# Kernel optimization log

Hardware: AMD Instinct MI355X
Metric: run time of the kernel (lower is better)

Reference implementation:

```python
import jax, jax.numpy as jnp
import numpy as np

HEADS = 8
HEAD_DIM = 32
DIM = 256        # embed_dim; inner_dim = HEADS*HEAD_DIM = 256
DEPTH = 2
MLP_DIM = 1024
GRID_H, GRID_W = 64, 64
CELL_DIM = 15    # pe(0) + in(3) + out(3) + hidden(9)
PE_IN = 3        # cell_pe_patch_dim + cell_in_patch_dim
UPDATE_DIM = 12  # cell_out(3) + hidden(9)
BATCH = 8


def layer_norm(x, g, b, eps=1e-5):
    m = jnp.mean(x, axis=-1, keepdims=True)
    v = jnp.var(x, axis=-1, keepdims=True)
    return (x - m) * jax.lax.rsqrt(v + eps) * g + b


def vit_positional_encoding(n, dim):
    pos = jnp.arange(n, dtype=jnp.float32)[:, None]
    div = jnp.exp(jnp.arange(0, dim, 2, dtype=jnp.float32) * (-np.log(10000.0) / dim))
    pe = jnp.zeros((n, dim), dtype=jnp.float32)
    pe = pe.at[:, 0::2].set(jnp.sin(pos * div)).at[:, 1::2].set(jnp.cos(pos * div))
    return pe[None]  # [1, n, dim]


def localize(x, H, W):
    # x: [b, heads, n, d] with n = H*W. Gather circular 3x3 neighbourhood per position
    # (equivalent to circular pad + one-hot conv in the torch LocalizeAttention).
    b, nh, n, d = x.shape
    y = x.reshape(b, nh, H, W, d)
    neigh = [jnp.roll(y, (1 - ki, 1 - kj), axis=(2, 3)) for ki in range(3) for kj in range(3)]
    return jnp.stack(neigh, axis=4).reshape(b, nh, n, 9, d)  # [b, h, n, 9, d]


def setup_inputs() -> dict:
    key = jax.random.key(0)
    ks = jax.random.split(key, 20)
    d = {}
    d['cells'] = jax.random.normal(ks[0], (BATCH, CELL_DIM, GRID_H, GRID_W), dtype=jnp.float32)
    s = 0.02
    d['We'] = jax.random.normal(ks[1], (CELL_DIM, DIM), jnp.float32) * s
    d['be'] = jnp.zeros((DIM,), jnp.float32)
    d['ln1_g'] = jnp.ones((DEPTH, DIM), jnp.float32)
    d['ln1_b'] = jnp.zeros((DEPTH, DIM), jnp.float32)
    d['Wqkv'] = jax.random.normal(ks[2], (DEPTH, DIM, 3 * HEADS * HEAD_DIM), jnp.float32) * s
    d['Wo'] = jax.random.normal(ks[3], (DEPTH, HEADS * HEAD_DIM, DIM), jnp.float32) * s
    d['bo'] = jnp.zeros((DEPTH, DIM), jnp.float32)
    d['ln2_g'] = jnp.ones((DEPTH, DIM), jnp.float32)
    d['ln2_b'] = jnp.zeros((DEPTH, DIM), jnp.float32)
    d['W1'] = jax.random.normal(ks[4], (DEPTH, DIM, MLP_DIM), jnp.float32) * s
    d['b1'] = jnp.zeros((DEPTH, MLP_DIM), jnp.float32)
    d['W2'] = jax.random.normal(ks[5], (DEPTH, MLP_DIM, DIM), jnp.float32) * s
    d['b2'] = jnp.zeros((DEPTH, DIM), jnp.float32)
    d['lnh_g'] = jnp.ones((DIM,), jnp.float32)
    d['lnh_b'] = jnp.zeros((DIM,), jnp.float32)
    # NOTE: torch zero-inits mlp_head; we use small random weights so the output is nontrivial.
    d['Wh'] = jax.random.normal(ks[6], (DIM, UPDATE_DIM), jnp.float32) * s
    d['bh'] = jnp.zeros((UPDATE_DIM,), jnp.float32)
    return d


def reference(cells, We, be, ln1_g, ln1_b, Wqkv, Wo, bo, ln2_g, ln2_b,
              W1, b1, W2, b2, lnh_g, lnh_b, Wh, bh):
    b, c, H, W = cells.shape
    n = H * W
    x = cells.reshape(b, c, n).transpose(0, 2, 1)           # b n c
    x = x @ We + be                                         # cell_to_embedding
    x = x + vit_positional_encoding(n, x.shape[-1])
    scale = HEAD_DIM ** -0.5
    for l in range(DEPTH):
        y = layer_norm(x, ln1_g[l], ln1_b[l])
        qkv = y @ Wqkv[l]                                   # b n 3*inner
        q, k, v = jnp.split(qkv, 3, axis=-1)
        split_heads = lambda t: t.reshape(b, n, HEADS, HEAD_DIM).transpose(0, 2, 1, 3)
        q, k, v = split_heads(q), split_heads(k), split_heads(v)  # b h n d
        kl = localize(k, H, W)                              # b h n 9 d
        vl = localize(v, H, W)
        dots = jnp.einsum('bhnd,bhnkd->bhnk', q, kl) * scale
        attn = jax.nn.softmax(dots, axis=-1)
        out = jnp.einsum('bhnk,bhnkd->bhnd', attn, vl)
        out = out.transpose(0, 2, 1, 3).reshape(b, n, HEADS * HEAD_DIM)
        x = out @ Wo[l] + bo[l] + x                         # attention + residual
        y = layer_norm(x, ln2_g[l], ln2_b[l])
        y = jax.nn.gelu(y @ W1[l] + b1[l], approximate=False) @ W2[l] + b2[l]
        x = x + y                                           # ffn + residual
    upd = layer_norm(x, lnh_g, lnh_b) @ Wh + bh             # b n UPDATE_DIM
    upd = upd.transpose(0, 2, 1).reshape(b, UPDATE_DIM, H, W)
    # update_rate = 1.0 -> deterministic branch: cells[:, PE_IN:] + update
    updated = cells[:, PE_IN:] + upd
    return jnp.concatenate([cells[:, :PE_IN], updated], axis=1)
```

## Files before the change

kernel.cpp:

```cpp
#include <hip/hip_runtime.h>
#include <hip/hip_bf16.h>
#include <math.h>

#define HEADS 8
#define HEAD_DIM 32
#define DIM 256
#define MLP_DIM 1024
#define NTOK 4096
#define BATCH 8
#define M_TOK (BATCH*NTOK)
#define CELL_DIM 15
#define PE_IN 3
#define UPD 12
#define HME ((size_t)M_TOK*32)

typedef __attribute__((ext_vector_type(8))) short bf16x8;
typedef __attribute__((ext_vector_type(4))) float f32x4;

static __device__ __forceinline__ unsigned short f2bf(float f) {
    __hip_bfloat16 h = __float2bfloat16(f);
    union { __hip_bfloat16 h; unsigned short u; } cv; cv.h = h; return cv.u;
}
static __device__ __forceinline__ void gload_lds16(const unsigned short* g, unsigned short* l) {
    __builtin_amdgcn_global_load_lds(
        (const __attribute__((address_space(1))) void*)g,
        (__attribute__((address_space(3))) void*)l, 16, 0, 0);
}
static __device__ __forceinline__ float gelu_fast(float v) {
    return v / (1.f + __expf(-1.59576912f * (v + 0.044715f * v * v * v)));
}

__global__ __launch_bounds__(256) void k_embed(const float* __restrict__ cells,
        const float* __restrict__ We, const float* __restrict__ be,
        const float* __restrict__ g, const float* __restrict__ bln,
        float* __restrict__ x, unsigned short* __restrict__ y) {
    __shared__ float red[8];
    int tok = blockIdx.x;
    int d = threadIdx.x;
    int b = tok >> 12, n = tok & 4095;
    const float* cb = cells + (size_t)b * CELL_DIM * NTOK + n;
    float acc = 0.f;
#pragma unroll
    for (int c = 0; c < CELL_DIM; ++c)
        acc += cb[c * NTOK] * We[c * DIM + d];
    int i = d >> 1;
    float freq = expf(-logf(10000.f) * (float)(2 * i) / (float)DIM);
    float ph = (float)n * freq;
    float pe = (d & 1) ? cosf(ph) : sinf(ph);
    float v = acc + be[d] + pe;
    x[(size_t)tok * DIM + d] = v;
    float s = v, ss = v * v;
#pragma unroll
    for (int off = 32; off; off >>= 1) { s += __shfl_xor(s, off); ss += __shfl_xor(ss, off); }
    int wave = d >> 6, lane = d & 63;
    if (lane == 0) { red[wave] = s; red[4 + wave] = ss; }
    __syncthreads();
    float stot = red[0] + red[1] + red[2] + red[3];
    float sstot = red[4] + red[5] + red[6] + red[7];
    float mean = stot * (1.f / DIM);
    float rstd = rsqrtf(sstot * (1.f / DIM) - mean * mean + 1e-5f);
    y[(size_t)tok * DIM + d] = f2bf((v - mean) * rstd * g[d] + bln[d]);
}

__global__ __launch_bounds__(256) void k_prep(const float* __restrict__ Wqkv,
        const float* __restrict__ Wo, const float* __restrict__ W1,
        const float* __restrict__ W2, const float* __restrict__ Wh,
        unsigned short* __restrict__ wT) {
    int seg = blockIdx.y;
    int idx = blockIdx.x * 256 + threadIdx.x;
    if (seg == 8) {
        if (idx >= 16 * 256) return;
        int u = idx >> 8, k = idx & 255;
        wT[1572864 + idx] = (u < UPD) ? f2bf(Wh[(size_t)k * UPD + u]) : (unsigned short)0;
        return;
    }
    int l = seg >> 2, mat = seg & 3;
    const float* src; int kwSh, Nw; size_t ooff;
    switch (mat) {
        case 0: src = Wqkv + (size_t)l * 196608; kwSh = 8;  Nw = 768;  ooff = (size_t)l * 786432 + 0;      break;
        case 1: src = Wo   + (size_t)l * 65536;  kwSh = 8;  Nw = 256;  ooff = (size_t)l * 786432 + 196608; break;
        case 2: src = W1   + (size_t)l * 262144; kwSh = 8;  Nw = 1024; ooff = (size_t)l * 786432 + 262144; break;
        default:src = W2   + (size_t)l * 262144; kwSh = 10; Nw = 256;  ooff = (size_t)l * 786432 + 524288; break;
    }
    int Kw = 1 << kwSh;
    if (idx >= Kw * Nw) return;
    int n = idx >> kwSh, k = idx & (Kw - 1);
    wT[ooff + idx] = f2bf(src[(size_t)k * Nw + n]);
}

template<int EPI>
__global__ __launch_bounds__(256) void k_mgemm(const unsigned short* __restrict__ A,
        const unsigned short* __restrict__ BT, const float* __restrict__ bias,
        void* __restrict__ Cout, int M, int N, int K, int NT) {
    __shared__ unsigned short As[2][128 * 32];
    __shared__ unsigned short Bs[2][128 * 32];
    int bid = blockIdx.x;
    int cpx = gridDim.x >> 3;
    int sb = (bid & 7) * cpx + (bid >> 3);
    int mt = sb / NT, nt = sb - mt * NT;
    int m0 = mt * 128, n0 = nt * 128;
    int t = threadIdx.x;
    int lane = t & 63, w = t >> 6;
    int wm = (w >> 1) * 64, wn = (w & 1) * 64;
    f32x4 acc[4][4] = {};
    int srow = t >> 2;
    int cg = (t & 3) ^ ((srow >> 1) & 3);
    const unsigned short* aBase = A  + (size_t)(m0 + srow) * K + cg * 8;
    const unsigned short* bBase = BT + (size_t)(n0 + srow) * K + cg * 8;
    int fr = lane & 15, kb8 = lane >> 4;

    auto stage = [&](int buf, int k0) {
        gload_lds16(aBase + k0,          &As[buf][t * 8]);
        gload_lds16(aBase + 64 * K + k0, &As[buf][2048 + t * 8]);
        gload_lds16(bBase + k0,          &Bs[buf][t * 8]);
        gload_lds16(bBase + 64 * K + k0, &Bs[buf][2048 + t * 8]);
    };
    auto compute = [&](int buf) {
        bf16x8 af[4], bfv[4];
#pragma unroll
        for (int i = 0; i < 4; ++i) {
            int r_ = wm + i * 16 + fr;
            af[i] = *(const bf16x8*)&As[buf][r_ * 32 + ((kb8 ^ ((r_ >> 1) & 3)) << 3)];
        }
#pragma unroll
        for (int j = 0; j < 4; ++j) {
            int r_ = wn + j * 16 + fr;
            bfv[j] = *(const bf16x8*)&Bs[buf][r_ * 32 + ((kb8 ^ ((r_ >> 1) & 3)) << 3)];
        }
#pragma unroll
        for (int i = 0; i < 4; ++i)
#pragma unroll
            for (int j = 0; j < 4; ++j)
                acc[i][j] = __builtin_amdgcn_mfma_f32_16x16x32_bf16(bfv[j], af[i], acc[i][j], 0, 0, 0);
    };

    stage(0, 0);
    __syncthreads();
    int cur = 0;
    for (int k0 = 32; k0 < K; k0 += 32) {
        stage(cur ^ 1, k0);
        compute(cur);
        __syncthreads();
        cur ^= 1;
    }
    compute(cur);

    int mcol = lane & 15, nq = (lane >> 4) * 4;
#pragma unroll
    for (int i = 0; i < 4; ++i) {
        int m = m0 + wm + i * 16 + mcol;
#pragma unroll
        for (int j = 0; j < 4; ++j) {
            int ng = n0 + wn + j * 16 + nq;
            if (EPI == 3) {
                int type = ng >> 8, rem = ng & 255;
                ushort4 pk;
                pk.x = f2bf(acc[i][j][0]); pk.y = f2bf(acc[i][j][1]);
                pk.z = f2bf(acc[i][j][2]); pk.w = f2bf(acc[i][j][3]);
                *(ushort4*)((unsigned short*)Cout +
                    (size_t)(type * 8 + (rem >> 5)) * HME + (size_t)m * 32 + (rem & 31)) = pk;
            } else {
                float4 b4 = *(const float4*)&bias[ng];
                ushort4 pk;
                pk.x = f2bf(gelu_fast(acc[i][j][0] + b4.x));
                pk.y = f2bf(gelu_fast(acc[i][j][1] + b4.y));
                pk.z = f2bf(gelu_fast(acc[i][j][2] + b4.z));
                pk.w = f2bf(gelu_fast(acc[i][j][3] + b4.w));
                *(ushort4*)((unsigned short*)Cout + (size_t)m * N + ng) = pk;
            }
        }
    }
}

template<int ALAYOUT>
__global__ __launch_bounds__(512) void k_mgemm_ln(const unsigned short* __restrict__ A,
        const unsigned short* __restrict__ BT, const float* __restrict__ bias,
        const float* __restrict__ g, const float* __restrict__ bln,
        float* __restrict__ x, unsigned short* __restrict__ y, int K) {
    __shared__ unsigned short As[2][128 * 32];
    __shared__ unsigned short Bs[2][256 * 32];
    __shared__ float sred[128 * 4];
    __shared__ float ssred[128 * 4];
    __shared__ float msr[128 * 2];
    int t = threadIdx.x;
    int lane = t & 63, w = t >> 6;
    int wm = (w >> 2) * 64, wn = (w & 3) * 64, wnq = w & 3;
    int m0 = blockIdx.x * 128;

    f32x4 acc[4][4] = {};
    int srow = t >> 2;
    int cg = (t & 3) ^ ((srow >> 1) & 3);
    const unsigned short* aBase = (ALAYOUT == 0)
        ? A + (size_t)(m0 + srow) * K + cg * 8
        : A + (size_t)(m0 + srow) * 32 + cg * 8;
    const unsigned short* bBase = BT + (size_t)srow * K + cg * 8;
    int fr = lane & 15, kb8 = lane >> 4;

    auto stage = [&](int buf, int k0) {
        const unsigned short* aSrc = (ALAYOUT == 0) ? aBase + k0 : aBase + (size_t)(k0 >> 5) * HME;
        gload_lds16(aSrc,                 &As[buf][t * 8]);
        gload_lds16(bBase + k0,           &Bs[buf][t * 8]);
        gload_lds16(bBase + 128 * K + k0, &Bs[buf][4096 + t * 8]);
    };
    auto compute = [&](int buf) {
        bf16x8 af[4], bfv[4];
#pragma unroll
        for (int i = 0; i < 4; ++i) {
            int r_ = wm + i * 16 + fr;
            af[i] = *(const bf16x8*)&As[buf][r_ * 32 + ((kb8 ^ ((r_ >> 1) & 3)) << 3)];
        }
#pragma unroll
        for (int j = 0; j < 4; ++j) {
            int r_ = wn + j * 16 + fr;
            bfv[j] = *(const bf16x8*)&Bs[buf][r_ * 32 + ((kb8 ^ ((r_ >> 1) & 3)) << 3)];
        }
#pragma unroll
        for (int i = 0; i < 4; ++i)
#pragma unroll
            for (int j = 0; j < 4; ++j)
                acc[i][j] = __builtin_amdgcn_mfma_f32_16x16x32_bf16(bfv[j], af[i], acc[i][j], 0, 0, 0);
    };

    stage(0, 0);
    __syncthreads();
    int cur = 0;
    for (int k0 = 32; k0 < K; k0 += 32) {
        stage(cur ^ 1, k0);
        compute(cur);
        __syncthreads();
        cur ^= 1;
    }
    compute(cur);

    int mloc = lane & 15, nq = (lane >> 4) * 4;
#pragma unroll
    for (int i = 0; i < 4; ++i) {
        int gm = m0 + wm + i * 16 + mloc;
        float s = 0.f, ss = 0.f;
#pragma unroll
        for (int j = 0; j < 4; ++j) {
            int nb = wn + j * 16 + nq;
            float4 b4 = *(const float4*)&bias[nb];
            float4 x4 = *(const float4*)&x[(size_t)gm * DIM + nb];
            acc[i][j][0] += b4.x + x4.x;
            acc[i][j][1] += b4.y + x4.y;
            acc[i][j][2] += b4.z + x4.z;
            acc[i][j][3] += b4.w + x4.w;
#pragma unroll
            for (int r = 0; r < 4; ++r) { float v = acc[i][j][r]; s += v; ss += v * v; }
        }
        s += __shfl_xor(s, 16); ss += __shfl_xor(ss, 16);
        s += __shfl_xor(s, 32); ss += __shfl_xor(ss, 32);
        if (lane < 16) {
            int row = wm + i * 16 + lane;
            sred[row * 4 + wnq] = s;
            ssred[row * 4 + wnq] = ss;
        }
    }
    __syncthreads();
    if (t < 128) {
        float s = sred[t * 4] + sred[t * 4 + 1] + sred[t * 4 + 2] + sred[t * 4 + 3];
        float ss = ssred[t * 4] + ssred[t * 4 + 1] + ssred[t * 4 + 2] + ssred[t * 4 + 3];
        float mean = s * (1.f / DIM);
        float var = ss * (1.f / DIM) - mean * mean;
        msr[t * 2] = mean;
        msr[t * 2 + 1] = rsqrtf(var + 1e-5f);
    }
    __syncthreads();
#pragma unroll
    for (int i = 0; i < 4; ++i) {
        int row = wm + i * 16 + mloc;
        int gm = m0 + row;
        float mean = msr[row * 2], rstd = msr[row * 2 + 1];
#pragma unroll
        for (int j = 0; j < 4; ++j) {
            int nb = wn + j * 16 + nq;
            float4 gv4 = *(const float4*)&g[nb];
            float4 bb4 = *(const float4*)&bln[nb];
            float4 xo;
            xo.x = acc[i][j][0]; xo.y = acc[i][j][1];
            xo.z = acc[i][j][2]; xo.w = acc[i][j][3];
            *(float4*)&x[(size_t)gm * DIM + nb] = xo;
            ushort4 yv;
            yv.x = f2bf((xo.x - mean) * rstd * gv4.x + bb4.x);
            yv.y = f2bf((xo.y - mean) * rstd * gv4.y + bb4.y);
            yv.z = f2bf((xo.z - mean) * rstd * gv4.z + bb4.z);
            yv.w = f2bf((xo.w - mean) * rstd * gv4.w + bb4.w);
            *(ushort4*)&y[(size_t)gm * DIM + nb] = yv;
        }
    }
}

__global__ __launch_bounds__(256) void k_attn(const unsigned short* __restrict__ qkvH,
        unsigned short* __restrict__ attnH) {
    int t = threadIdx.x;
    int h = t >> 5, tl = t & 31;
    int tok = blockIdx.x * 32 + tl;
    int b = tok >> 12, n = tok & 4095;
    int r = n >> 6, c = n & 63;

    float q[32];
    {
        const uint4* u = (const uint4*)(qkvH + (size_t)h * HME + (size_t)tok * 32);
#pragma unroll
        for (int i = 0; i < 4; ++i) {
            uint4 x4 = u[i];
            unsigned wv[4] = {x4.x, x4.y, x4.z, x4.w};
#pragma unroll
            for (int wj = 0; wj < 4; ++wj) {
                q[i * 8 + wj * 2]     = __uint_as_float(wv[wj] << 16);
                q[i * 8 + wj * 2 + 1] = __uint_as_float(wv[wj] & 0xffff0000u);
            }
        }
    }
    int nts[9];
    float dots[9];
    const unsigned short* kbase = qkvH + (size_t)(8 + h) * HME;
#pragma unroll
    for (int ki = 0; ki < 3; ++ki)
#pragma unroll
        for (int kj = 0; kj < 3; ++kj) {
            int rr = (r + ki - 1) & 63, cc = (c + kj - 1) & 63;
            int nt = (b << 12) + (rr << 6) + cc;
            nts[ki * 3 + kj] = nt;
            const uint4* u = (const uint4*)(kbase + (size_t)nt * 32);
            float acc = 0.f;
#pragma unroll
            for (int i = 0; i < 4; ++i) {
                uint4 x4 = u[i];
                unsigned wv[4] = {x4.x, x4.y, x4.z, x4.w};
#pragma unroll
                for (int wj = 0; wj < 4; ++wj) {
                    acc += __uint_as_float(wv[wj] << 16)        * q[i * 8 + wj * 2];
                    acc += __uint_as_float(wv[wj] & 0xffff0000u) * q[i * 8 + wj * 2 + 1];
                }
            }
            dots[ki * 3 + kj] = acc * 0.17677669529f;
        }
    float m = dots[0];
#pragma unroll
    for (int j = 1; j < 9; ++j) m = fmaxf(m, dots[j]);
    float sum = 0.f;
#pragma unroll
    for (int j = 0; j < 9; ++j) { dots[j] = __expf(dots[j] - m); sum += dots[j]; }
    float inv = 1.f / sum;
    float o[32] = {};
    const unsigned short* vbase = qkvH + (size_t)(16 + h) * HME;
#pragma unroll
    for (int j = 0; j < 9; ++j) {
        float wgt = dots[j] * inv;
        const uint4* u = (const uint4*)(vbase + (size_t)nts[j] * 32);
#pragma unroll
        for (int i = 0; i < 4; ++i) {
            uint4 x4 = u[i];
            unsigned wv[4] = {x4.x, x4.y, x4.z, x4.w};
#pragma unroll
            for (int wj = 0; wj < 4; ++wj) {
                o[i * 8 + wj * 2]     += wgt * __uint_as_float(wv[wj] << 16);
                o[i * 8 + wj * 2 + 1] += wgt * __uint_as_float(wv[wj] & 0xffff0000u);
            }
        }
    }
    uint4 st[4];
    unsigned* sw = (unsigned*)st;
#pragma unroll
    for (int i = 0; i < 16; ++i)
        sw[i] = (unsigned)f2bf(o[2 * i]) | ((unsigned)f2bf(o[2 * i + 1]) << 16);
    uint4* od = (uint4*)(attnH + (size_t)h * HME + (size_t)tok * 32);
#pragma unroll
    for (int i = 0; i < 4; ++i) od[i] = st[i];
}

__global__ __launch_bounds__(256) void k_headgemv(const unsigned short* __restrict__ y,
        const unsigned short* __restrict__ WhT, float* __restrict__ Cg) {
    int t = threadIdx.x, lane = t & 63, w = t >> 6;
    int m0 = blockIdx.x * 64 + w * 16;
    int fr = lane & 15, kb = (lane >> 4) * 8;
    f32x4 acc = {};
    const unsigned short* aRow = y + (size_t)(m0 + fr) * DIM + kb;
    const unsigned short* bRow = WhT + (size_t)fr * DIM + kb;
#pragma unroll
    for (int k0 = 0; k0 < DIM; k0 += 32) {
        bf16x8 a = *(const bf16x8*)(aRow + k0);
        bf16x8 bfr = *(const bf16x8*)(bRow + k0);
        acc = __builtin_amdgcn_mfma_f32_16x16x32_bf16(a, bfr, acc, 0, 0, 0);
    }
    int col = lane & 15, rowq = (lane >> 4) * 4;
#pragma unroll
    for (int r = 0; r < 4; ++r)
        Cg[(size_t)(m0 + rowq + r) * 16 + col] = acc[r];
}

__global__ __launch_bounds__(256) void k_assemble(const float* __restrict__ cells,
        const float* __restrict__ Cg, const float* __restrict__ bh,
        float* __restrict__ outp) {
    int idx = blockIdx.x * 256 + threadIdx.x;
    int total = BATCH * CELL_DIM * (NTOK / 4);
    if (idx >= total) return;
    int n4 = idx & 1023;
    int c = (idx >> 10) % CELL_DIM;
    int b = idx / (CELL_DIM * 1024);
    size_t ci = ((size_t)b * CELL_DIM + c) * NTOK + n4 * 4;
    float4 o = *(const float4*)(cells + ci);
    if (c >= PE_IN) {
        int u = c - PE_IN;
        float bias = bh[u];
        size_t tok = (size_t)b * NTOK + n4 * 4;
        o.x += Cg[(tok + 0) * 16 + u] + bias;
        o.y += Cg[(tok + 1) * 16 + u] + bias;
        o.z += Cg[(tok + 2) * 16 + u] + bias;
        o.w += Cg[(tok + 3) * 16 + u] + bias;
    }
    *(float4*)(outp + ci) = o;
}

extern "C" void kernel_launch(void* const* d_in, const int* in_sizes, int n_in,
                              void* d_out, int out_size, void* d_ws, size_t ws_size,
                              hipStream_t stream) {
    const float* cells = (const float*)d_in[0];
    const float* We    = (const float*)d_in[1];
    const float* be    = (const float*)d_in[2];
    const float* ln1_g = (const float*)d_in[3];
    const float* ln1_b = (const float*)d_in[4];
    const float* Wqkv  = (const float*)d_in[5];
    const float* Wo    = (const float*)d_in[6];
    const float* bo    = (const float*)d_in[7];
    const float* ln2_g = (const float*)d_in[8];
    const float* ln2_b = (const float*)d_in[9];
    const float* W1    = (const float*)d_in[10];
    const float* b1    = (const float*)d_in[11];
    const float* W2    = (const float*)d_in[12];
    const float* b2    = (const float*)d_in[13];
    const float* lnh_g = (const float*)d_in[14];
    const float* lnh_b = (const float*)d_in[15];
    const float* Wh    = (const float*)d_in[16];
    const float* bh    = (const float*)d_in[17];
    float* outp = (float*)d_out;

    char* ws = (char*)d_ws;
    float* x = (float*)ws;
    unsigned short* y = (unsigned short*)(ws + 33554432);
    unsigned short* scratch = (unsigned short*)(ws + 50331648);
    unsigned short* wT = (unsigned short*)(ws + 117440512);
    unsigned short* qkvH  = scratch;
    unsigned short* attnH = scratch + 24 * HME;
    unsigned short* hidden = scratch;
    float* Cg = (float*)scratch;

    k_prep<<<dim3(1024, 9), 256, 0, stream>>>(Wqkv, Wo, W1, W2, Wh, wT);
    k_embed<<<M_TOK, 256, 0, stream>>>(cells, We, be, ln1_g, ln1_b, x, y);
    for (int l = 0; l < 2; ++l) {
        const unsigned short* wL = wT + (size_t)l * 786432;
        const float* gN = (l == 0) ? ln1_g + DIM : lnh_g;
        const float* bN = (l == 0) ? ln1_b + DIM : lnh_b;
        k_mgemm<3><<<1536, 256, 0, stream>>>(
            y, wL + 0, nullptr, qkvH, M_TOK, 768, DIM, 6);
        k_attn<<<M_TOK / 32, 256, 0, stream>>>(qkvH, attnH);
        k_mgemm_ln<1><<<M_TOK / 128, 512, 0, stream>>>(
            attnH, wL + 196608, bo + l * DIM, ln2_g + l * DIM, ln2_b + l * DIM, x, y, DIM);
        k_mgemm<1><<<2048, 256, 0, stream>>>(
            y, wL + 262144, b1 + l * MLP_DIM, hidden, M_TOK, MLP_DIM, DIM, 8);
        k_mgemm_ln<0><<<M_TOK / 128, 512, 0, stream>>>(
            hidden, wL + 524288, b2 + l * DIM, gN, bN, x, y, MLP_DIM);
    }
    k_headgemv<<<M_TOK / 64, 256, 0, stream>>>(y, wT + 1572864, Cg);
    k_assemble<<<(BATCH * CELL_DIM * (NTOK / 4) + 255) / 256, 256, 0, stream>>>(cells, Cg, bh, outp);
}
```

Baseline: 393.7 us.

## Triple-buffer GEMM LDS staging with prefetch distance two and partial vmcnt waits

Both MFMA GEMM kernels move from double to triple LDS buffering. Global-to-LDS loads are now issued two K-steps ahead, and each barrier uses a partial s_waitcnt vmcnt so only the oldest stage has to land before compute continues. This is meant to hide global-load latency that the previous full __syncthreads wait exposed. In exchange it uses 1.5x the LDS, which can lower occupancy, especially for the 512-thread LN kernel, and it relies on hand-tuned vmcnt counts being correct.

```diff
diff --git a/kernel.cpp b/kernel.cpp
--- a/kernel.cpp
+++ b/kernel.cpp
@@ -92,8 +92,8 @@
 __global__ __launch_bounds__(256) void k_mgemm(const unsigned short* __restrict__ A,
         const unsigned short* __restrict__ BT, const float* __restrict__ bias,
         void* __restrict__ Cout, int M, int N, int K, int NT) {
-    __shared__ unsigned short As[2][128 * 32];
-    __shared__ unsigned short Bs[2][128 * 32];
+    __shared__ unsigned short As[3][128 * 32];
+    __shared__ unsigned short Bs[3][128 * 32];
     int bid = blockIdx.x;
     int cpx = gridDim.x >> 3;
     int sb = (bid & 7) * cpx + (bid >> 3);
@@ -110,22 +110,26 @@
     int fr = lane & 15, kb8 = lane >> 4;
 
     auto stage = [&](int buf, int k0) {
-        gload_lds16(aBase + k0,          &As[buf][t * 8]);
-        gload_lds16(aBase + 64 * K + k0, &As[buf][2048 + t * 8]);
-        gload_lds16(bBase + k0,          &Bs[buf][t * 8]);
-        gload_lds16(bBase + 64 * K + k0, &Bs[buf][2048 + t * 8]);
+        unsigned short* a = &As[0][0] + buf * 4096;
+        unsigned short* b = &Bs[0][0] + buf * 4096;
+        gload_lds16(aBase + k0,          a + t * 8);
+        gload_lds16(aBase + 64 * K + k0, a + 2048 + t * 8);
+        gload_lds16(bBase + k0,          b + t * 8);
+        gload_lds16(bBase + 64 * K + k0, b + 2048 + t * 8);
     };
     auto compute = [&](int buf) {
+        const unsigned short* a = &As[0][0] + buf * 4096;
+        const unsigned short* b = &Bs[0][0] + buf * 4096;
         bf16x8 af[4], bfv[4];
 #pragma unroll
         for (int i = 0; i < 4; ++i) {
             int r_ = wm + i * 16 + fr;
-            af[i] = *(const bf16x8*)&As[buf][r_ * 32 + ((kb8 ^ ((r_ >> 1) & 3)) << 3)];
+            af[i] = *(const bf16x8*)&a[r_ * 32 + ((kb8 ^ ((r_ >> 1) & 3)) << 3)];
         }
 #pragma unroll
         for (int j = 0; j < 4; ++j) {
             int r_ = wn + j * 16 + fr;
-            bfv[j] = *(const bf16x8*)&Bs[buf][r_ * 32 + ((kb8 ^ ((r_ >> 1) & 3)) << 3)];
+            bfv[j] = *(const bf16x8*)&b[r_ * 32 + ((kb8 ^ ((r_ >> 1) & 3)) << 3)];
         }
 #pragma unroll
         for (int i = 0; i < 4; ++i)
@@ -134,14 +138,26 @@
                 acc[i][j] = __builtin_amdgcn_mfma_f32_16x16x32_bf16(bfv[j], af[i], acc[i][j], 0, 0, 0);
     };
 
+    int nk = K >> 5;
     stage(0, 0);
-    __syncthreads();
+    stage(1, 32);
+    asm volatile("s_waitcnt vmcnt(4)" ::: "memory");
+    __builtin_amdgcn_s_barrier();
+    __builtin_amdgcn_sched_barrier(0);
     int cur = 0;
-    for (int k0 = 32; k0 < K; k0 += 32) {
-        stage(cur ^ 1, k0);
+    for (int k = 0; k < nk - 1; ++k) {
+        int pre = k + 2;
+        if (pre < nk) {
+            int preBuf = cur + 2; if (preBuf >= 3) preBuf -= 3;
+            stage(preBuf, pre * 32);
+        }
         compute(cur);
-        __syncthreads();
-        cur ^= 1;
+        __builtin_amdgcn_sched_barrier(0);
+        if (pre < nk) asm volatile("s_waitcnt vmcnt(4)" ::: "memory");
+        else          asm volatile("s_waitcnt vmcnt(0)" ::: "memory");
+        __builtin_amdgcn_s_barrier();
+        __builtin_amdgcn_sched_barrier(0);
+        ++cur; if (cur >= 3) cur -= 3;
     }
     compute(cur);
 
@@ -177,8 +193,8 @@
         const unsigned short* __restrict__ BT, const float* __restrict__ bias,
         const float* __restrict__ g, const float* __restrict__ bln,
         float* __restrict__ x, unsigned short* __restrict__ y, int K) {
-    __shared__ unsigned short As[2][128 * 32];
-    __shared__ unsigned short Bs[2][256 * 32];
+    __shared__ unsigned short As[3][128 * 32];
+    __shared__ unsigned short Bs[3][256 * 32];
     __shared__ float sred[128 * 4];
     __shared__ float ssred[128 * 4];
     __shared__ float msr[128 * 2];
@@ -197,22 +213,26 @@
     int fr = lane & 15, kb8 = lane >> 4;
 
     auto stage = [&](int buf, int k0) {
+        unsigned short* as_ = &As[0][0] + buf * 4096;
+        unsigned short* bs_ = &Bs[0][0] + buf * 8192;
         const unsigned short* aSrc = (ALAYOUT == 0) ? aBase + k0 : aBase + (size_t)(k0 >> 5) * HME;
-        gload_lds16(aSrc,                 &As[buf][t * 8]);
-        gload_lds16(bBase + k0,           &Bs[buf][t * 8]);
-        gload_lds16(bBase + 128 * K + k0, &Bs[buf][4096 + t * 8]);
+        gload_lds16(aSrc,                 as_ + t * 8);
+        gload_lds16(bBase + k0,           bs_ + t * 8);
+        gload_lds16(bBase + 128 * K + k0, bs_ + 4096 + t * 8);
     };
     auto compute = [&](int buf) {
+        const unsigned short* as_ = &As[0][0] + buf * 4096;
+        const unsigned short* bs_ = &Bs[0][0] + buf * 8192;
         bf16x8 af[4], bfv[4];
 #pragma unroll
         for (int i = 0; i < 4; ++i) {
             int r_ = wm + i * 16 + fr;
-            af[i] = *(const bf16x8*)&As[buf][r_ * 32 + ((kb8 ^ ((r_ >> 1) & 3)) << 3)];
+            af[i] = *(const bf16x8*)&as_[r_ * 32 + ((kb8 ^ ((r_ >> 1) & 3)) << 3)];
         }
 #pragma unroll
         for (int j = 0; j < 4; ++j) {
             int r_ = wn + j * 16 + fr;
-            bfv[j] = *(const bf16x8*)&Bs[buf][r_ * 32 + ((kb8 ^ ((r_ >> 1) & 3)) << 3)];
+            bfv[j] = *(const bf16x8*)&bs_[r_ * 32 + ((kb8 ^ ((r_ >> 1) & 3)) << 3)];
         }
 #pragma unroll
         for (int i = 0; i < 4; ++i)
@@ -221,14 +241,26 @@
                 acc[i][j] = __builtin_amdgcn_mfma_f32_16x16x32_bf16(bfv[j], af[i], acc[i][j], 0, 0, 0);
     };
 
+    int nk = K >> 5;
     stage(0, 0);
-    __syncthreads();
+    stage(1, 32);
+    asm volatile("s_waitcnt vmcnt(3)" ::: "memory");
+    __builtin_amdgcn_s_barrier();
+    __builtin_amdgcn_sched_barrier(0);
     int cur = 0;
-    for (int k0 = 32; k0 < K; k0 += 32) {
-        stage(cur ^ 1, k0);
+    for (int k = 0; k < nk - 1; ++k) {
+        int pre = k + 2;
+        if (pre < nk) {
+            int preBuf = cur + 2; if (preBuf >= 3) preBuf -= 3;
+            stage(preBuf, pre * 32);
+        }
         compute(cur);
-        __syncthreads();
-        cur ^= 1;
+        __builtin_amdgcn_sched_barrier(0);
+        if (pre < nk) asm volatile("s_waitcnt vmcnt(3)" ::: "memory");
+        else          asm volatile("s_waitcnt vmcnt(0)" ::: "memory");
+        __builtin_amdgcn_s_barrier();
+        __builtin_amdgcn_sched_barrier(0);
+        ++cur; if (cur >= 3) cur -= 3;
     }
     compute(cur);
 
```

Result: no change. 387.4 us (-1.6%).
